# Kernel optimization log

Hardware: AMD Instinct MI355X
Metric: run time of the kernel (lower is better)

## Reference

```python
import jax, jax.numpy as jnp
import numpy as np

B, F, N = 16, 128, 20000  # batch, feature (edge==node==message size), num nodes
M = F  # message_size = edge_feature_size


def setup_inputs() -> dict:
    key = jax.random.key(0)
    ks = jax.random.split(key, 9)
    s = 1.0 / np.sqrt(F)
    return {
        "h_w": jax.random.normal(ks[0], (B, F, N), jnp.float32),
        "h_v": jax.random.normal(ks[1], (B, F), jnp.float32),
        "e_wv": jax.random.normal(ks[2], (B, F, N), jnp.float32),
        "W_e2m": jax.random.normal(ks[3], (M, F), jnp.float32) * s,
        "b_e2m": jax.random.normal(ks[4], (M,), jnp.float32) * s,
        "W_n2m": jax.random.normal(ks[5], (M, F), jnp.float32) * s,
        "b_n2m": jax.random.normal(ks[6], (M,), jnp.float32) * s,
        "W_resize": jax.random.normal(ks[7], (M, 3 * M), jnp.float32) * (1.0 / np.sqrt(3 * M)),
        "b_resize": jax.random.normal(ks[8], (M,), jnp.float32) * (1.0 / np.sqrt(3 * M)),
    }


def reference(h_w, h_v, e_wv, W_e2m, b_e2m, W_n2m, b_n2m, W_resize, b_resize):
    # Per-node loop vectorized over the node axis n.
    # tmp_msg = cat([e2m(e_wv[:,:,n]), n2m(h_w[:,:,n]), n2m(h_v)], dim=1)
    # message[:,:,n] = resize_m(tmp_msg)
    # Split W_resize into its three column blocks to avoid materializing the
    # [B, 3M, N] concat: resize(cat(a,b,c)) = Wa@a + Wb@b + Wc@c + b.
    Wa = W_resize[:, :M]          # acts on e2m output
    Wb = W_resize[:, M:2 * M]     # acts on n2m(h_w)
    Wc = W_resize[:, 2 * M:]      # acts on n2m(h_v)

    em = jnp.einsum('bfn,mf->bmn', e_wv, W_e2m) + b_e2m[:, None]   # [B,M,N]
    nw = jnp.einsum('bfn,mf->bmn', h_w, W_n2m) + b_n2m[:, None]    # [B,M,N]
    nv = h_v @ W_n2m.T + b_n2m                                      # [B,M]

    msg = (jnp.einsum('bmn,km->bkn', em, Wa)
           + jnp.einsum('bmn,km->bkn', nw, Wb)
           + ((nv @ Wc.T) + b_resize)[:, :, None])                  # [B,M,N]
    return msg
```

## Files before the change

### kernel.cpp

```cpp
#include <hip/hip_runtime.h>
#include <hip/hip_bf16.h>

typedef __attribute__((ext_vector_type(8))) short bf16x8;
typedef __attribute__((ext_vector_type(4))) float f32x4;

#define B_DIM 16
#define F_DIM 128
#define N_DIM 20000
#define M_DIM 128
#define NW 32
#define NSUB 2
#define TILES_PER_B 625
#define NBLK (16 * TILES_PER_B)
#define LDS_F32_MAT 16384
#define LDS_BF16_OFF 32768
#define LDS_BF16_MAT 8192

#define AS1 __attribute__((address_space(1)))
#define AS3 __attribute__((address_space(3)))

static __device__ inline unsigned short f2bf(float x) {
    union { float f; unsigned u; } v; v.f = x;
    unsigned r = v.u + 0x7fffu + ((v.u >> 16) & 1u);
    return (unsigned short)(r >> 16);
}

__global__ __launch_bounds__(256) void precompute_mats(
    const float* __restrict__ W_rs,
    const float* __restrict__ W_e2m,
    const float* __restrict__ W_n2m,
    unsigned short* __restrict__ wsA,
    unsigned short* __restrict__ wsB)
{
    int idx = blockIdx.x * 256 + threadIdx.x;
    int k = idx >> 7;
    int f = idx & 127;
    float a = 0.f, b = 0.f;
    for (int m = 0; m < 128; ++m) {
        a += W_rs[k * 384 + m]       * W_e2m[m * 128 + f];
        b += W_rs[k * 384 + 128 + m] * W_n2m[m * 128 + f];
    }
    int mt = k >> 4, row = k & 15;
    int c = f >> 5, kk = f & 31;
    int lane = ((kk >> 3) << 4) | row;
    int j = kk & 7;
    int off = ((mt * 4 + c) * 64 + lane) * 8 + j;
    wsA[off] = f2bf(a);
    wsB[off] = f2bf(b);
}

__global__ __launch_bounds__(128) void precompute_bias(
    const float* __restrict__ W_rs,
    const float* __restrict__ h_v,
    const float* __restrict__ b_e2m,
    const float* __restrict__ b_n2m,
    const float* __restrict__ b_rs,
    const float* __restrict__ W_n2m,
    float* __restrict__ bias)
{
    __shared__ float nv_s[128];
    int b = blockIdx.x;
    int t = threadIdx.x;
    {
        float nv = b_n2m[t];
        for (int f = 0; f < 128; ++f)
            nv += h_v[b * 128 + f] * W_n2m[t * 128 + f];
        nv_s[t] = nv;
    }
    __syncthreads();
    {
        float acc = b_rs[t];
        for (int m = 0; m < 128; ++m) {
            acc += W_rs[t * 384 + m]       * b_e2m[m];
            acc += W_rs[t * 384 + 128 + m] * b_n2m[m];
            acc += W_rs[t * 384 + 256 + m] * nv_s[m];
        }
        bias[b * 128 + t] = acc;
    }
}

__global__ __launch_bounds__(256) void msg_main(
    const float* __restrict__ e_wv,
    const float* __restrict__ h_w,
    const unsigned short* __restrict__ wsA,
    const unsigned short* __restrict__ wsB,
    const float* __restrict__ bias,
    float* __restrict__ out)
{
    __shared__ __align__(16) unsigned char smem[49152];

    int tid = threadIdx.x;
    int w   = tid >> 6;
    int l   = tid & 63;
    int blk0 = blockIdx.x;
    int blk  = (blk0 & 7) * (NBLK / 8) + (blk0 >> 3);
    int b   = blk / TILES_PER_B;
    int n0  = (blk - b * TILES_PER_B) * NW;

    const float* eb = e_wv + (size_t)b * (F_DIM * (size_t)N_DIM) + n0;
    const float* wb = h_w  + (size_t)b * (F_DIM * (size_t)N_DIM) + n0;

    {
        int qsw = ((l & 7) ^ (l >> 3)) * 4;
        int fl  = l >> 3;
#pragma unroll
        for (int i = 0; i < 4; ++i) {
            int f_base = i * 32 + w * 8;
            unsigned char* ld_e = smem + f_base * 128;
            unsigned char* ld_w = smem + LDS_F32_MAT + f_base * 128;
            const float* ge = eb + (size_t)(f_base + fl) * N_DIM + qsw;
            const float* gw = wb + (size_t)(f_base + fl) * N_DIM + qsw;
            __builtin_amdgcn_global_load_lds((const AS1 unsigned*)ge, (AS3 unsigned*)ld_e, 16, 0, 0);
            __builtin_amdgcn_global_load_lds((const AS1 unsigned*)gw, (AS3 unsigned*)ld_w, 16, 0, 0);
        }
    }
    __syncthreads();

    {
        int m    = tid >> 7;
        int u    = tid & 127;
        int fp   = u >> 1;
        int half = u & 1;
        const unsigned char* fsrc = smem + m * LDS_F32_MAT;
        unsigned char* bdst = smem + LDS_BF16_OFF + m * LDS_BF16_MAT;
        int f0 = 2 * fp, f1 = 2 * fp + 1;
        int x0 = f0 & 7, x1 = f1 & 7;
#pragma unroll
        for (int j = 0; j < 4; ++j) {
            int q = half * 4 + j;
            f32x4 a = *(const f32x4*)(fsrc + f0 * 128 + (q ^ x0) * 16);
            f32x4 c = *(const f32x4*)(fsrc + f1 * 128 + (q ^ x1) * 16);
#pragma unroll
            for (int e = 0; e < 4; ++e) {
                int n = q * 4 + e;
                unsigned pk = (unsigned)f2bf(a[e]) | ((unsigned)f2bf(c[e]) << 16);
                unsigned off = (unsigned)(n * 256) +
                               ((unsigned)(fp * 4) ^ (unsigned)((n & 7) << 4));
                *(unsigned*)(bdst + off) = pk;
            }
        }
    }
    __syncthreads();

    int ln = l & 15, g = l >> 4;
    f32x4 acc[2][NSUB];
#pragma unroll
    for (int mtL = 0; mtL < 2; ++mtL)
#pragma unroll
        for (int ns = 0; ns < NSUB; ++ns) acc[mtL][ns] = (f32x4)(0.f);

    const bf16x8* Af = (const bf16x8*)wsA;
    const bf16x8* Bf = (const bf16x8*)wsB;
    const unsigned char* ldse = smem + LDS_BF16_OFF;
    const unsigned char* ldsw = smem + LDS_BF16_OFF + LDS_BF16_MAT;
    unsigned rbase = (unsigned)(ln * 256);
    unsigned rx = (unsigned)((ln & 7) << 4);

#pragma unroll
    for (int c = 0; c < 4; ++c) {
        bf16x8 a0 = Af[((2 * w + 0) * 4 + c) * 64 + l];
        bf16x8 a1 = Af[((2 * w + 1) * 4 + c) * 64 + l];
        bf16x8 b0 = Bf[((2 * w + 0) * 4 + c) * 64 + l];
        bf16x8 b1 = Bf[((2 * w + 1) * 4 + c) * 64 + l];
        unsigned fbyte = (unsigned)((c * 32 + g * 8) * 2) ^ rx;
#pragma unroll
        for (int ns = 0; ns < NSUB; ++ns) {
            bf16x8 xe = *(const bf16x8*)(ldse + ns * 4096 + rbase + fbyte);
            bf16x8 xw = *(const bf16x8*)(ldsw + ns * 4096 + rbase + fbyte);
            acc[0][ns] = __builtin_amdgcn_mfma_f32_16x16x32_bf16(a0, xe, acc[0][ns], 0, 0, 0);
            acc[0][ns] = __builtin_amdgcn_mfma_f32_16x16x32_bf16(b0, xw, acc[0][ns], 0, 0, 0);
            acc[1][ns] = __builtin_amdgcn_mfma_f32_16x16x32_bf16(a1, xe, acc[1][ns], 0, 0, 0);
            acc[1][ns] = __builtin_amdgcn_mfma_f32_16x16x32_bf16(b1, xw, acc[1][ns], 0, 0, 0);
        }
    }

    const f32x4* bias4 = (const f32x4*)(bias + b * 128);
    float* O = out + (size_t)b * (M_DIM * (size_t)N_DIM) + n0 + ln;
#pragma unroll
    for (int mtL = 0; mtL < 2; ++mtL) {
        int mt = 2 * w + mtL;
        f32x4 bb = bias4[mt * 4 + g];
#pragma unroll
        for (int ns = 0; ns < NSUB; ++ns) {
#pragma unroll
            for (int r = 0; r < 4; ++r) {
                int k = mt * 16 + g * 4 + r;
                O[(size_t)k * N_DIM + ns * 16] = acc[mtL][ns][r] + bb[r];
            }
        }
    }
}

extern "C" void kernel_launch(void* const* d_in, const int* in_sizes, int n_in,
                              void* d_out, int out_size, void* d_ws, size_t ws_size,
                              hipStream_t stream) {
    const float* h_w   = (const float*)d_in[0];
    const float* h_v   = (const float*)d_in[1];
    const float* e_wv  = (const float*)d_in[2];
    const float* W_e2m = (const float*)d_in[3];
    const float* b_e2m = (const float*)d_in[4];
    const float* W_n2m = (const float*)d_in[5];
    const float* b_n2m = (const float*)d_in[6];
    const float* W_rs  = (const float*)d_in[7];
    const float* b_rs  = (const float*)d_in[8];
    float* out = (float*)d_out;

    unsigned short* wsA = (unsigned short*)d_ws;
    unsigned short* wsB = wsA + 128 * 128;
    float* bias = (float*)((char*)d_ws + 65536);

    precompute_mats<<<64, 256, 0, stream>>>(W_rs, W_e2m, W_n2m, wsA, wsB);
    precompute_bias<<<16, 128, 0, stream>>>(W_rs, h_v, b_e2m, b_n2m, b_rs, W_n2m, bias);
    msg_main<<<NBLK, 256, 0, stream>>>(e_wv, h_w, wsA, wsB, bias, out);
}
```

Measured before the change: 139.7 us.

## Make msg kernel persistent with double-buffered async tile loads

Replaces the one-tile-per-block launch with a persistent grid of 500 blocks, each processing 20 consecutive tiles. Global-to-LDS DMA for tile t+2 is issued while tile t is computed, using two fp32 staging buffers and manual waitcnt/barrier sequencing. The bf16 weight fragments are hoisted into registers once per block. This aims to hide load latency and remove per-block launch and weight-reload overhead. The cost is more LDS per block, fewer blocks in flight, and wait counts that also include output stores, which may serialize.

```diff
diff --git a/kernel.cpp b/kernel.cpp
--- a/kernel.cpp
+++ b/kernel.cpp
@@ -4,17 +4,17 @@
 typedef __attribute__((ext_vector_type(8))) short bf16x8;
 typedef __attribute__((ext_vector_type(4))) float f32x4;
 
-#define B_DIM 16
 #define F_DIM 128
 #define N_DIM 20000
 #define M_DIM 128
 #define NW 32
-#define NSUB 2
 #define TILES_PER_B 625
-#define NBLK (16 * TILES_PER_B)
-#define LDS_F32_MAT 16384
-#define LDS_BF16_OFF 32768
-#define LDS_BF16_MAT 8192
+#define NT 20
+#define GRID 500
+#define F32_TILE 32768
+#define F32_MAT 16384
+#define BF16_OFF 65536
+#define BF16_MAT 8192
 
 #define AS1 __attribute__((address_space(1)))
 #define AS3 __attribute__((address_space(3)))
@@ -79,7 +79,7 @@
     }
 }
 
-__global__ __launch_bounds__(256) void msg_main(
+__global__ __launch_bounds__(256, 2) void msg_main(
     const float* __restrict__ e_wv,
     const float* __restrict__ h_w,
     const unsigned short* __restrict__ wsA,
@@ -87,108 +87,138 @@
     const float* __restrict__ bias,
     float* __restrict__ out)
 {
-    __shared__ __align__(16) unsigned char smem[49152];
+    __shared__ __align__(16) unsigned char smem[81920];
 
     int tid = threadIdx.x;
     int w   = tid >> 6;
     int l   = tid & 63;
-    int blk0 = blockIdx.x;
-    int blk  = (blk0 & 7) * (NBLK / 8) + (blk0 >> 3);
-    int b   = blk / TILES_PER_B;
-    int n0  = (blk - b * TILES_PER_B) * NW;
-
-    const float* eb = e_wv + (size_t)b * (F_DIM * (size_t)N_DIM) + n0;
-    const float* wb = h_w  + (size_t)b * (F_DIM * (size_t)N_DIM) + n0;
-
-    {
-        int qsw = ((l & 7) ^ (l >> 3)) * 4;
-        int fl  = l >> 3;
+    unsigned base = (unsigned)blockIdx.x * NT;
+
+    const bf16x8* Af = (const bf16x8*)wsA;
+    const bf16x8* Bf = (const bf16x8*)wsB;
+    bf16x8 A0[4], A1[4], B0[4], B1[4];
+#pragma unroll
+    for (int c = 0; c < 4; ++c) {
+        A0[c] = Af[((2 * w + 0) * 4 + c) * 64 + l];
+        A1[c] = Af[((2 * w + 1) * 4 + c) * 64 + l];
+        B0[c] = Bf[((2 * w + 0) * 4 + c) * 64 + l];
+        B1[c] = Bf[((2 * w + 1) * 4 + c) * 64 + l];
+    }
+
+    int fl = l >> 3, p = l & 7;
+    auto issue_dma = [&](unsigned tau, unsigned bufsel) {
+        unsigned bb = tau / TILES_PER_B;
+        unsigned n0 = (tau - bb * TILES_PER_B) * NW;
+        const float* eb = e_wv + (size_t)bb * (F_DIM * (size_t)N_DIM) + n0;
+        const float* wp = h_w  + (size_t)bb * (F_DIM * (size_t)N_DIM) + n0;
+        unsigned char* buf = smem + bufsel * F32_TILE;
 #pragma unroll
         for (int i = 0; i < 4; ++i) {
-            int f_base = i * 32 + w * 8;
-            unsigned char* ld_e = smem + f_base * 128;
-            unsigned char* ld_w = smem + LDS_F32_MAT + f_base * 128;
-            const float* ge = eb + (size_t)(f_base + fl) * N_DIM + qsw;
-            const float* gw = wb + (size_t)(f_base + fl) * N_DIM + qsw;
-            __builtin_amdgcn_global_load_lds((const AS1 unsigned*)ge, (AS3 unsigned*)ld_e, 16, 0, 0);
-            __builtin_amdgcn_global_load_lds((const AS1 unsigned*)gw, (AS3 unsigned*)ld_w, 16, 0, 0);
-        }
-    }
-    __syncthreads();
-
-    {
-        int m    = tid >> 7;
-        int u    = tid & 127;
-        int fp   = u >> 1;
-        int half = u & 1;
-        const unsigned char* fsrc = smem + m * LDS_F32_MAT;
-        unsigned char* bdst = smem + LDS_BF16_OFF + m * LDS_BF16_MAT;
+            int fb = i * 32 + w * 8;
+            int f  = fb + fl;
+            int g  = (f ^ (f >> 3)) & 7;
+            int col = (p ^ g) << 2;
+            __builtin_amdgcn_global_load_lds(
+                (const AS1 unsigned*)(eb + (size_t)f * N_DIM + col),
+                (AS3 unsigned*)(buf + fb * 128), 16, 0, 0);
+            __builtin_amdgcn_global_load_lds(
+                (const AS1 unsigned*)(wp + (size_t)f * N_DIM + col),
+                (AS3 unsigned*)(buf + F32_MAT + fb * 128), 16, 0, 0);
+        }
+    };
+
+    auto transform = [&](unsigned bufsel) {
+        const unsigned char* fsrc = smem + bufsel * F32_TILE + (tid >> 7) * F32_MAT;
+        unsigned char* bdst = smem + BF16_OFF + (tid >> 7) * BF16_MAT;
+        int u = tid & 127;
+        int fp = u >> 1, half = u & 1;
         int f0 = 2 * fp, f1 = 2 * fp + 1;
-        int x0 = f0 & 7, x1 = f1 & 7;
+        int g0 = (f0 ^ (f0 >> 3)) & 7, g1 = (f1 ^ (f1 >> 3)) & 7;
 #pragma unroll
         for (int j = 0; j < 4; ++j) {
             int q = half * 4 + j;
-            f32x4 a = *(const f32x4*)(fsrc + f0 * 128 + (q ^ x0) * 16);
-            f32x4 c = *(const f32x4*)(fsrc + f1 * 128 + (q ^ x1) * 16);
+            f32x4 a = *(const f32x4*)(fsrc + f0 * 128 + ((q ^ g0) << 4));
+            f32x4 c = *(const f32x4*)(fsrc + f1 * 128 + ((q ^ g1) << 4));
 #pragma unroll
             for (int e = 0; e < 4; ++e) {
                 int n = q * 4 + e;
                 unsigned pk = (unsigned)f2bf(a[e]) | ((unsigned)f2bf(c[e]) << 16);
                 unsigned off = (unsigned)(n * 256) +
-                               ((unsigned)(fp * 4) ^ (unsigned)((n & 7) << 4));
+                               (((unsigned)(fp * 4)) ^ ((unsigned)((n & 7) << 4)));
                 *(unsigned*)(bdst + off) = pk;
             }
         }
-    }
-    __syncthreads();
+    };
+
+    issue_dma(base + 0, 0);
+    issue_dma(base + 1, 1);
+    asm volatile("s_waitcnt vmcnt(8)" ::: "memory");
+    __builtin_amdgcn_s_barrier();
+    transform(0);
+    asm volatile("s_waitcnt lgkmcnt(0)" ::: "memory");
+    __builtin_amdgcn_s_barrier();
 
     int ln = l & 15, g = l >> 4;
-    f32x4 acc[2][NSUB];
-#pragma unroll
-    for (int mtL = 0; mtL < 2; ++mtL)
-#pragma unroll
-        for (int ns = 0; ns < NSUB; ++ns) acc[mtL][ns] = (f32x4)(0.f);
-
-    const bf16x8* Af = (const bf16x8*)wsA;
-    const bf16x8* Bf = (const bf16x8*)wsB;
-    const unsigned char* ldse = smem + LDS_BF16_OFF;
-    const unsigned char* ldsw = smem + LDS_BF16_OFF + LDS_BF16_MAT;
     unsigned rbase = (unsigned)(ln * 256);
     unsigned rx = (unsigned)((ln & 7) << 4);
-
-#pragma unroll
-    for (int c = 0; c < 4; ++c) {
-        bf16x8 a0 = Af[((2 * w + 0) * 4 + c) * 64 + l];
-        bf16x8 a1 = Af[((2 * w + 1) * 4 + c) * 64 + l];
-        bf16x8 b0 = Bf[((2 * w + 0) * 4 + c) * 64 + l];
-        bf16x8 b1 = Bf[((2 * w + 1) * 4 + c) * 64 + l];
-        unsigned fbyte = (unsigned)((c * 32 + g * 8) * 2) ^ rx;
-#pragma unroll
-        for (int ns = 0; ns < NSUB; ++ns) {
-            bf16x8 xe = *(const bf16x8*)(ldse + ns * 4096 + rbase + fbyte);
-            bf16x8 xw = *(const bf16x8*)(ldsw + ns * 4096 + rbase + fbyte);
-            acc[0][ns] = __builtin_amdgcn_mfma_f32_16x16x32_bf16(a0, xe, acc[0][ns], 0, 0, 0);
-            acc[0][ns] = __builtin_amdgcn_mfma_f32_16x16x32_bf16(b0, xw, acc[0][ns], 0, 0, 0);
-            acc[1][ns] = __builtin_amdgcn_mfma_f32_16x16x32_bf16(a1, xe, acc[1][ns], 0, 0, 0);
-            acc[1][ns] = __builtin_amdgcn_mfma_f32_16x16x32_bf16(b1, xw, acc[1][ns], 0, 0, 0);
-        }
-    }
-
-    const f32x4* bias4 = (const f32x4*)(bias + b * 128);
-    float* O = out + (size_t)b * (M_DIM * (size_t)N_DIM) + n0 + ln;
-#pragma unroll
-    for (int mtL = 0; mtL < 2; ++mtL) {
-        int mt = 2 * w + mtL;
-        f32x4 bb = bias4[mt * 4 + g];
-#pragma unroll
-        for (int ns = 0; ns < NSUB; ++ns) {
-#pragma unroll
-            for (int r = 0; r < 4; ++r) {
-                int k = mt * 16 + g * 4 + r;
-                O[(size_t)k * N_DIM + ns * 16] = acc[mtL][ns][r] + bb[r];
+    const unsigned char* ldse = smem + BF16_OFF;
+    const unsigned char* ldsw = smem + BF16_OFF + BF16_MAT;
+
+#pragma unroll 1
+    for (int t = 0; t < NT; ++t) {
+        unsigned tau = base + t;
+        unsigned bb = tau / TILES_PER_B;
+        unsigned n0 = (tau - bb * TILES_PER_B) * NW;
+
+        const float* bp = bias + bb * 128;
+        f32x4 bv0 = *(const f32x4*)(bp + (2 * w + 0) * 16 + g * 4);
+        f32x4 bv1 = *(const f32x4*)(bp + (2 * w + 1) * 16 + g * 4);
+
+        int t2 = t + 2; if (t2 >= NT) t2 -= NT;
+        issue_dma(base + t2, (unsigned)(t & 1));
+
+        f32x4 acc[2][2];
+#pragma unroll
+        for (int mtL = 0; mtL < 2; ++mtL)
+#pragma unroll
+            for (int ns = 0; ns < 2; ++ns) acc[mtL][ns] = (f32x4)(0.f);
+#pragma unroll
+        for (int c = 0; c < 4; ++c) {
+            unsigned fbyte = (unsigned)((c * 32 + g * 8) * 2) ^ rx;
+#pragma unroll
+            for (int ns = 0; ns < 2; ++ns) {
+                bf16x8 xe = *(const bf16x8*)(ldse + ns * 4096 + rbase + fbyte);
+                bf16x8 xw = *(const bf16x8*)(ldsw + ns * 4096 + rbase + fbyte);
+                acc[0][ns] = __builtin_amdgcn_mfma_f32_16x16x32_bf16(A0[c], xe, acc[0][ns], 0, 0, 0);
+                acc[0][ns] = __builtin_amdgcn_mfma_f32_16x16x32_bf16(B0[c], xw, acc[0][ns], 0, 0, 0);
+                acc[1][ns] = __builtin_amdgcn_mfma_f32_16x16x32_bf16(A1[c], xe, acc[1][ns], 0, 0, 0);
+                acc[1][ns] = __builtin_amdgcn_mfma_f32_16x16x32_bf16(B1[c], xw, acc[1][ns], 0, 0, 0);
             }
         }
-    }
+
+        asm volatile("s_waitcnt vmcnt(8)" ::: "memory");
+        asm volatile("s_waitcnt lgkmcnt(0)" ::: "memory");
+        __builtin_amdgcn_s_barrier();
+
+        if (t < NT - 1) transform((unsigned)((t + 1) & 1));
+        asm volatile("s_waitcnt lgkmcnt(0)" ::: "memory");
+        __builtin_amdgcn_s_barrier();
+
+        float* O = out + (size_t)bb * (M_DIM * (size_t)N_DIM) + n0 + ln;
+#pragma unroll
+        for (int mtL = 0; mtL < 2; ++mtL) {
+            f32x4 bv = mtL ? bv1 : bv0;
+            int mt = 2 * w + mtL;
+#pragma unroll
+            for (int ns = 0; ns < 2; ++ns)
+#pragma unroll
+                for (int r = 0; r < 4; ++r)
+                    O[(size_t)(mt * 16 + g * 4 + r) * N_DIM + ns * 16] =
+                        acc[mtL][ns][r] + bv[r];
+        }
+    }
+
+    asm volatile("s_waitcnt vmcnt(0)" ::: "memory");
 }
 
 extern "C" void kernel_launch(void* const* d_in, const int* in_sizes, int n_in,
@@ -211,5 +241,5 @@
 
     precompute_mats<<<64, 256, 0, stream>>>(W_rs, W_e2m, W_n2m, wsA, wsB);
     precompute_bias<<<16, 128, 0, stream>>>(W_rs, h_v, b_e2m, b_n2m, b_rs, W_n2m, bias);
-    msg_main<<<NBLK, 256, 0, stream>>>(e_wv, h_w, wsA, wsB, bias, out);
-}
+    msg_main<<<GRID, 256, 0, stream>>>(e_wv, h_w, wsA, wsB, bias, out);
+}
```

Result: faster. 134.4 us (-3.8%).
